# Kernel tuning notes

Measured on AMD Instinct MI355X. Metric: run time of the kernel, lower is better.

## Reference

```python
import jax, jax.numpy as jnp
import numpy as np

# plane_axes buffer from the torch module (permutation matrices)
PLANE_AXES = jnp.array([[[0, 1, 0], [1, 0, 0], [0, 0, 1]],
                        [[0, 0, 1], [1, 0, 0], [0, 1, 0]],
                        [[0, 1, 0], [0, 0, 1], [1, 0, 0]]], dtype=jnp.float32)

M = 1_000_000
C = 32
R = 512


def setup_inputs() -> dict:
    key = jax.random.key(0)
    k1, k2 = jax.random.split(key)
    # query points uniform in [-1, 1]^3 (grid_sample coordinate convention)
    xyz = jax.random.uniform(k1, (M, 3), dtype=jnp.float32) * 2.0 - 1.0
    triplane = jax.random.normal(k2, (1, 3, C, R, R), dtype=jnp.float32) * 0.05
    return {"xyz": xyz, "triplane": triplane, "oid": 0}


def _grid_sample_plane(img, gx, gy):
    """Bilinear grid_sample, align_corners=True, padding_mode='zeros'.
    img: [C, H, W]; gx, gy: [M] normalized coords in [-1, 1] (x -> W, y -> H).
    Returns [C, M]."""
    _, H, W = img.shape
    x = (gx + 1.0) * 0.5 * (W - 1)  # align_corners=True unnormalization
    y = (gy + 1.0) * 0.5 * (H - 1)
    x0 = jnp.floor(x)
    y0 = jnp.floor(y)
    x1 = x0 + 1.0
    y1 = y0 + 1.0
    wx1 = x - x0
    wx0 = 1.0 - wx1
    wy1 = y - y0
    wy0 = 1.0 - wy1

    def corner(xi, yi, w):
        valid = (xi >= 0) & (xi <= W - 1) & (yi >= 0) & (yi <= H - 1)
        xi_c = jnp.clip(xi, 0, W - 1).astype(jnp.int32)
        yi_c = jnp.clip(yi, 0, H - 1).astype(jnp.int32)
        vals = img[:, yi_c, xi_c]  # [C, M] gather
        return vals * (w * valid)[None, :]

    return (corner(x0, y0, wx0 * wy0) + corner(x1, y0, wx1 * wy0)
            + corner(x0, y1, wx0 * wy1) + corner(x1, y1, wx1 * wy1))


def reference(xyz, triplane, oid):
    # project_onto_planes: xyz [M,3] -> projections [3, M, 2]
    inv_planes = jnp.linalg.inv(PLANE_AXES)           # [3, 3, 3]
    proj = jnp.einsum('mk,pkj->pmj', xyz, inv_planes)[..., :2]  # [3, M, 2]
    planes = triplane[oid]                            # [3, C, R, R]
    # grid coords: last dim is (x, y) per torch grid_sample convention
    sampled = jax.vmap(_grid_sample_plane)(planes, proj[..., 0], proj[..., 1])  # [3, C, M]
    # permute(0,3,2,1).reshape(3,M,C).sum(0) -> [M, C]
    return sampled.sum(0).T
```

## Files before the change

### kernel.cpp

```cpp
#include <hip/hip_runtime.h>
#include <hip/hip_bf16.h>


#define RRTP 262144
#define CTP  32
#define NB   512
#define SORT_P 4096
#define TPBLK 3072
#define PLANE_B (RRTP * 64)

typedef float        f32x4 __attribute__((ext_vector_type(4)));
typedef unsigned int u32;
typedef u32          u32x4 __attribute__((ext_vector_type(4)));

__device__ __forceinline__ u32 part3b(u32 v) {
    return (v & 1) | ((v & 2) << 2) | ((v & 4) << 4);
}
__device__ __forceinline__ u32 morton9(float px, float py, float pz) {
    int qx = max(0, min(7, (int)((px + 1.0f) * 4.0f)));
    int qy = max(0, min(7, (int)((py + 1.0f) * 4.0f)));
    int qz = max(0, min(7, (int)((pz + 1.0f) * 4.0f)));
    return part3b((u32)qx) | (part3b((u32)qy) << 1) | (part3b((u32)qz) << 2);
}

__global__ __launch_bounds__(256) void tp_fused(const float* __restrict__ in,
                                                u32* __restrict__ texels,
                                                const float* __restrict__ xyz,
                                                u32* __restrict__ hist,
                                                const int* __restrict__ oid, int Mtot) {
    __shared__ float tile[256][33];
    const int t = threadIdx.x;

    if (blockIdx.x < TPBLK) {
        const int b     = blockIdx.x;
        const int plane = b >> 10;
        const int rr0   = (b & 1023) << 8;

        const float* src = in + (size_t)oid[0] * (3u * CTP * RRTP)
                              + (size_t)plane * (CTP * RRTP) + rr0 + t;
        #pragma unroll
        for (int c = 0; c < 32; ++c)
            tile[t][c] = src[(size_t)c * RRTP];
        __syncthreads();

        u32* dst = texels + (size_t)plane * ((size_t)RRTP * 16) + (size_t)rr0 * 16;
        const int cp = t & 15;
        #pragma unroll
        for (int k = 0; k < 16; ++k) {
            const int r = (k << 4) + (t >> 4);
            const float f0 = tile[r][cp * 2];
            const float f1 = tile[r][cp * 2 + 1];
            const u32 lo = (u32)__bfloat16_as_ushort(__float2bfloat16(f0));
            const u32 hi = (u32)__bfloat16_as_ushort(__float2bfloat16(f1));
            dst[(size_t)r * 16 + cp] = (hi << 16) | lo;
        }
    } else {
        u32* cnt = (u32*)&tile[0][0];
        const int b = blockIdx.x - TPBLK;
        cnt[t] = 0u; cnt[t + 256] = 0u;
        __syncthreads();
        const int base_m = b * SORT_P;
        #pragma unroll
        for (int i = 0; i < 16; ++i) {
            const int m = base_m + i * 256 + t;
            if (m < Mtot) {
                const u32 k = morton9(xyz[3 * m], xyz[3 * m + 1], xyz[3 * m + 2]);
                atomicAdd(&cnt[k], 1u);
            }
        }
        __syncthreads();
        hist[b * NB + t] = cnt[t];
        hist[b * NB + t + 256] = cnt[t + 256];
    }
}

__global__ __launch_bounds__(512) void tp_scanB(u32* __restrict__ hist,
                                                u32* __restrict__ bucket_base, int nblk) {
    const int k = threadIdx.x;
    u32 run = 0;
    #pragma unroll 8
    for (int b = 0; b < nblk; ++b) {
        const u32 v = hist[b * NB + k];
        hist[b * NB + k] = run;
        run += v;
    }
    __shared__ u32 sA[NB], sB[NB];
    sA[k] = run;
    int par = 0;
    for (int off = 1; off < NB; off <<= 1) {
        __syncthreads();
        u32* src = par ? sB : sA;
        u32* dst = par ? sA : sB;
        dst[k] = src[k] + ((k >= off) ? src[k - off] : 0u);
        par ^= 1;
    }
    __syncthreads();
    const u32 incl = (par ? sB : sA)[k];
    bucket_base[k] = incl - run;
}

__global__ __launch_bounds__(256) void tp_scatter_blk(const float* __restrict__ xyz,
                                                      const u32* __restrict__ hist,
                                                      const u32* __restrict__ bucket_base,
                                                      f32x4* __restrict__ sorted, int Mtot) {
    __shared__ u32 goff[NB];
    __shared__ u32 sA[NB], sB[NB];
    __shared__ f32x4 rec[SORT_P];
    __shared__ unsigned short lkey[SORT_P];
    const int t = threadIdx.x, b = blockIdx.x;
    const int base_m = b * SORT_P;

    sA[t] = 0u; sA[t + 256] = 0u;
    goff[t]       = bucket_base[t]       + hist[b * NB + t];
    goff[t + 256] = bucket_base[t + 256] + hist[b * NB + t + 256];
    __syncthreads();

    float xs[16], ys[16], zs[16]; u32 ks[16], rs[16];
    #pragma unroll
    for (int i = 0; i < 16; ++i) {
        const int m = base_m + i * 256 + t;
        const bool v = (m < Mtot);
        float px = 0.f, py = 0.f, pz = 0.f;
        if (v) { px = xyz[3 * m]; py = xyz[3 * m + 1]; pz = xyz[3 * m + 2]; }
        const u32 key = morton9(px, py, pz);
        xs[i] = px; ys[i] = py; zs[i] = pz;
        ks[i] = v ? key : 0xffffffffu;
        rs[i] = v ? atomicAdd(&sA[key], 1u) : 0u;
    }
    __syncthreads();

    const u32 c0 = sA[t], c1 = sA[t + 256];
    int par = 0;
    for (int off = 1; off < NB; off <<= 1) {
        u32* src = par ? sB : sA;
        u32* dst = par ? sA : sB;
        const u32 a0 = src[t]       + ((t >= off)       ? src[t - off]       : 0u);
        const u32 a1 = src[t + 256] + ((t + 256 >= off) ? src[t + 256 - off] : 0u);
        dst[t] = a0; dst[t + 256] = a1;
        par ^= 1;
        __syncthreads();
    }
    u32* incl = par ? sB : sA;
    const u32 lb0 = incl[t] - c0, lb1 = incl[t + 256] - c1;
    __syncthreads();
    sA[t] = lb0; sA[t + 256] = lb1;
    goff[t] -= lb0; goff[t + 256] -= lb1;
    __syncthreads();

    #pragma unroll
    for (int i = 0; i < 16; ++i) {
        if (ks[i] != 0xffffffffu) {
            const u32 pos = sA[ks[i]] + rs[i];
            f32x4 r = {xs[i], ys[i], zs[i],
                       __uint_as_float((u32)(base_m + i * 256 + t))};
            rec[pos] = r;
            lkey[pos] = (unsigned short)ks[i];
        }
    }
    __syncthreads();

    const int nv = min(SORT_P, Mtot - base_m);
    #pragma unroll
    for (int i = 0; i < 16; ++i) {
        const int s = i * 256 + t;
        if (s < nv) {
            const u32 k2 = lkey[s];
            sorted[goff[k2] + s] = rec[s];
        }
    }
}

__global__ __launch_bounds__(256) void tp_sample_sorted(const f32x4* __restrict__ sorted,
                                                        const u32* __restrict__ tp,
                                                        float* __restrict__ out,
                                                        int Mtot, int nwg) {
    __shared__ float srow[64][36];
    __shared__ u32   smid[64];

    const int bid = blockIdx.x;
    const int qc = nwg >> 3, rc = nwg & 7;
    const int xcd = bid & 7, j = bid >> 3;
    const int wg = ((xcd < rc) ? xcd * (qc + 1) : rc * (qc + 1) + (xcd - rc) * qc) + j;

    const int tid = wg * 256 + threadIdx.x;
    const int sp = tid >> 2;
    const u32 oq = (u32)((tid & 3) << 4);
    const int lp = threadIdx.x >> 2;

    if (sp < Mtot) {
        const f32x4 pt = sorted[sp];
        const float px = pt.x, py = pt.y, pz = pt.z;
        const u32 m = __float_as_uint(pt.w);

        const float gxs[3] = {py, pz, py};
        const float gys[3] = {px, px, pz};

        f32x4 alo = {0.f, 0.f, 0.f, 0.f};
        f32x4 ahi = {0.f, 0.f, 0.f, 0.f};

        const char* tpc = (const char*)tp;

        #pragma unroll
        for (int p = 0; p < 3; ++p) {
            const float xf = (gxs[p] + 1.0f) * (0.5f * 511.0f);
            const float yf = (gys[p] + 1.0f) * (0.5f * 511.0f);
            const float x0f = floorf(xf), y0f = floorf(yf);
            float wx1 = xf - x0f, wy1 = yf - y0f;
            float wx0 = 1.0f - wx1, wy0 = 1.0f - wy1;

            int x0 = (int)x0f, y0 = (int)y0f;
            int x1 = x0 + 1,   y1 = y0 + 1;
            if (x1 > 511) { x1 = 511; wx1 = 0.0f; }
            if (y1 > 511) { y1 = 511; wy1 = 0.0f; }
            x0 = max(0, min(511, x0));
            y0 = max(0, min(511, y0));

            const u32 ry0 = ((u32)y0 << 15), ry1 = ((u32)y1 << 15);
            const u32 cx0 = ((u32)x0 << 6)  + oq, cx1 = ((u32)x1 << 6) + oq;
            const char* base_p = tpc + (size_t)p * PLANE_B;

            const u32x4 v00 = *(const u32x4*)(base_p + (ry0 + cx0));
            const u32x4 v01 = *(const u32x4*)(base_p + (ry0 + cx1));
            const u32x4 v10 = *(const u32x4*)(base_p + (ry1 + cx0));
            const u32x4 v11 = *(const u32x4*)(base_p + (ry1 + cx1));

            const float w00 = wy0 * wx0, w01 = wy0 * wx1;
            const float w10 = wy1 * wx0, w11 = wy1 * wx1;

            #pragma unroll
            for (int i = 0; i < 4; ++i) {
                const float l00 = __uint_as_float(v00[i] << 16), h00 = __uint_as_float(v00[i] & 0xffff0000u);
                const float l01 = __uint_as_float(v01[i] << 16), h01 = __uint_as_float(v01[i] & 0xffff0000u);
                const float l10 = __uint_as_float(v10[i] << 16), h10 = __uint_as_float(v10[i] & 0xffff0000u);
                const float l11 = __uint_as_float(v11[i] << 16), h11 = __uint_as_float(v11[i] & 0xffff0000u);
                alo[i] = fmaf(w00, l00, fmaf(w01, l01, fmaf(w10, l10, fmaf(w11, l11, alo[i]))));
                ahi[i] = fmaf(w00, h00, fmaf(w01, h01, fmaf(w10, h10, fmaf(w11, h11, ahi[i]))));
            }
        }

        float* sr = &srow[lp][oq >> 1];
        sr[0] = alo[0]; sr[1] = ahi[0]; sr[2] = alo[1]; sr[3] = ahi[1];
        sr[4] = alo[2]; sr[5] = ahi[2]; sr[6] = alo[3]; sr[7] = ahi[3];
        smid[lp] = m;
    }
    __syncthreads();

    const int pc = threadIdx.x & 7;
    const int pb = threadIdx.x >> 3;
    const int spbase = wg * 64;
    #pragma unroll
    for (int jj = 0; jj < 2; ++jj) {
        const int lpt = pb + jj * 32;
        if (spbase + lpt < Mtot) {
            const u32 mj = smid[lpt];
            const f32x4 v = *(const f32x4*)&srow[lpt][pc << 2];
            __builtin_nontemporal_store(v, (f32x4*)(out + ((size_t)mj << 5) + (pc << 2)));
        }
    }
}

__global__ __launch_bounds__(256) void tp_sample_direct(const float* __restrict__ xyz,
                                                        const float* __restrict__ tpl,
                                                        const int* __restrict__ oid,
                                                        float* __restrict__ out,
                                                        int Mtot) {
    const int tid = blockIdx.x * 256 + threadIdx.x;
    const int m = tid >> 5;
    if (m >= Mtot) return;
    const int c = tid & 31;
    const float px = xyz[m * 3 + 0], py = xyz[m * 3 + 1], pz = xyz[m * 3 + 2];
    const float gxs[3] = {py, pz, py};
    const float gys[3] = {px, px, pz};
    const float* base = tpl + (size_t)oid[0] * (3u * CTP * RRTP);
    float acc = 0.f;
    #pragma unroll
    for (int p = 0; p < 3; ++p) {
        const float xf = (gxs[p] + 1.0f) * (0.5f * 511.0f);
        const float yf = (gys[p] + 1.0f) * (0.5f * 511.0f);
        const float x0f = floorf(xf), y0f = floorf(yf);
        float wx1 = xf - x0f, wy1 = yf - y0f;
        float wx0 = 1.0f - wx1, wy0 = 1.0f - wy1;
        int x0 = (int)x0f, y0 = (int)y0f;
        int x1 = x0 + 1,   y1 = y0 + 1;
        if (x1 > 511) { x1 = 511; wx1 = 0.0f; }
        if (y1 > 511) { y1 = 511; wy1 = 0.0f; }
        x0 = max(0, min(511, x0));
        y0 = max(0, min(511, y0));
        const float* img = base + ((size_t)p * CTP + c) * RRTP;
        acc += wy0 * (wx0 * img[(y0 << 9) + x0] + wx1 * img[(y0 << 9) + x1])
             + wy1 * (wx0 * img[(y1 << 9) + x0] + wx1 * img[(y1 << 9) + x1]);
    }
    out[((size_t)m << 5) + c] = acc;
}

extern "C" void kernel_launch(void* const* d_in, const int* in_sizes, int n_in,
                              void* d_out, int out_size, void* d_ws, size_t ws_size,
                              hipStream_t stream) {
    const float* xyz      = (const float*)d_in[0];
    const float* triplane = (const float*)d_in[1];
    const int*   oid      = (const int*)d_in[2];
    float*       out      = (float*)d_out;
    const int Mtot = in_sizes[0] / 3;
    const int nblk = (Mtot + SORT_P - 1) / SORT_P;

    const size_t hist_b   = 512 * 1024;
    const size_t bb_off   = hist_b;
    const size_t sorted_off = hist_b + 64 * 1024;
    const size_t sorted_b = (size_t)Mtot * 16;
    const size_t texel_off = sorted_off + sorted_b;
    const size_t texel_b  = (size_t)3 * RRTP * 16 * 4;
    const size_t ws_needed = texel_off + texel_b;

    if (ws_size >= ws_needed && (size_t)nblk * NB * 4 <= hist_b) {
        u32*   hist   = (u32*)d_ws;
        u32*   bbase  = (u32*)((char*)d_ws + bb_off);
        f32x4* sorted = (f32x4*)((char*)d_ws + sorted_off);
        u32*   texels = (u32*)((char*)d_ws + texel_off);

        tp_fused<<<TPBLK + nblk, 256, 0, stream>>>(triplane, texels, xyz, hist, oid, Mtot);
        tp_scanB<<<1, 512, 0, stream>>>(hist, bbase, nblk);
        tp_scatter_blk<<<nblk, 256, 0, stream>>>(xyz, hist, bbase, sorted, Mtot);

        const int nwg = (Mtot * 4 + 255) / 256;
        tp_sample_sorted<<<nwg, 256, 0, stream>>>(sorted, texels, out, Mtot, nwg);
    } else {
        tp_sample_direct<<<(Mtot * 32 + 255) / 256, 256, 0, stream>>>(xyz, triplane, oid, out, Mtot);
    }
}
```

Measured before the change: 135.8 us.

## Move triplane bf16 repack into the scatter kernel and halve sort block size

The triplane transpose/bf16 conversion now runs in the same launch as the per-block counting-sort scatter, not alongside the histogram pass. This keeps the serial histogram/scan phase short and lets the heavy repack overlap with the scatter. SORT_P is halved to 2048, giving more, lighter scatter blocks with a 40KB shared buffer reused across both roles. The cost is a larger histogram and a longer serial loop in the single-block scan (twice as many blocks).

```diff
diff --git a/kernel.cpp b/kernel.cpp
--- a/kernel.cpp
+++ b/kernel.cpp
@@ -5,7 +5,7 @@
 #define RRTP 262144
 #define CTP  32
 #define NB   512
-#define SORT_P 4096
+#define SORT_P 2048
 #define TPBLK 3072
 #define PLANE_B (RRTP * 64)
 
@@ -23,55 +23,24 @@
     return part3b((u32)qx) | (part3b((u32)qy) << 1) | (part3b((u32)qz) << 2);
 }
 
-__global__ __launch_bounds__(256) void tp_fused(const float* __restrict__ in,
-                                                u32* __restrict__ texels,
-                                                const float* __restrict__ xyz,
-                                                u32* __restrict__ hist,
-                                                const int* __restrict__ oid, int Mtot) {
-    __shared__ float tile[256][33];
-    const int t = threadIdx.x;
-
-    if (blockIdx.x < TPBLK) {
-        const int b     = blockIdx.x;
-        const int plane = b >> 10;
-        const int rr0   = (b & 1023) << 8;
-
-        const float* src = in + (size_t)oid[0] * (3u * CTP * RRTP)
-                              + (size_t)plane * (CTP * RRTP) + rr0 + t;
-        #pragma unroll
-        for (int c = 0; c < 32; ++c)
-            tile[t][c] = src[(size_t)c * RRTP];
-        __syncthreads();
-
-        u32* dst = texels + (size_t)plane * ((size_t)RRTP * 16) + (size_t)rr0 * 16;
-        const int cp = t & 15;
-        #pragma unroll
-        for (int k = 0; k < 16; ++k) {
-            const int r = (k << 4) + (t >> 4);
-            const float f0 = tile[r][cp * 2];
-            const float f1 = tile[r][cp * 2 + 1];
-            const u32 lo = (u32)__bfloat16_as_ushort(__float2bfloat16(f0));
-            const u32 hi = (u32)__bfloat16_as_ushort(__float2bfloat16(f1));
-            dst[(size_t)r * 16 + cp] = (hi << 16) | lo;
-        }
-    } else {
-        u32* cnt = (u32*)&tile[0][0];
-        const int b = blockIdx.x - TPBLK;
-        cnt[t] = 0u; cnt[t + 256] = 0u;
-        __syncthreads();
-        const int base_m = b * SORT_P;
-        #pragma unroll
-        for (int i = 0; i < 16; ++i) {
-            const int m = base_m + i * 256 + t;
-            if (m < Mtot) {
-                const u32 k = morton9(xyz[3 * m], xyz[3 * m + 1], xyz[3 * m + 2]);
-                atomicAdd(&cnt[k], 1u);
-            }
-        }
-        __syncthreads();
-        hist[b * NB + t] = cnt[t];
-        hist[b * NB + t + 256] = cnt[t + 256];
-    }
+__global__ __launch_bounds__(256) void tp_hist_blk(const float* __restrict__ xyz,
+                                                   u32* __restrict__ hist, int Mtot) {
+    __shared__ u32 cnt[NB];
+    const int t = threadIdx.x, b = blockIdx.x;
+    cnt[t] = 0u; cnt[t + 256] = 0u;
+    __syncthreads();
+    const int base_m = b * SORT_P;
+    #pragma unroll
+    for (int i = 0; i < 8; ++i) {
+        const int m = base_m + i * 256 + t;
+        if (m < Mtot) {
+            const u32 k = morton9(xyz[3 * m], xyz[3 * m + 1], xyz[3 * m + 2]);
+            atomicAdd(&cnt[k], 1u);
+        }
+    }
+    __syncthreads();
+    hist[b * NB + t] = cnt[t];
+    hist[b * NB + t + 256] = cnt[t + 256];
 }
 
 __global__ __launch_bounds__(512) void tp_scanB(u32* __restrict__ hist,
@@ -99,73 +68,108 @@
     bucket_base[k] = incl - run;
 }
 
-__global__ __launch_bounds__(256) void tp_scatter_blk(const float* __restrict__ xyz,
-                                                      const u32* __restrict__ hist,
-                                                      const u32* __restrict__ bucket_base,
-                                                      f32x4* __restrict__ sorted, int Mtot) {
-    __shared__ u32 goff[NB];
-    __shared__ u32 sA[NB], sB[NB];
-    __shared__ f32x4 rec[SORT_P];
-    __shared__ unsigned short lkey[SORT_P];
-    const int t = threadIdx.x, b = blockIdx.x;
-    const int base_m = b * SORT_P;
-
-    sA[t] = 0u; sA[t + 256] = 0u;
-    goff[t]       = bucket_base[t]       + hist[b * NB + t];
-    goff[t + 256] = bucket_base[t + 256] + hist[b * NB + t + 256];
-    __syncthreads();
-
-    float xs[16], ys[16], zs[16]; u32 ks[16], rs[16];
-    #pragma unroll
-    for (int i = 0; i < 16; ++i) {
-        const int m = base_m + i * 256 + t;
-        const bool v = (m < Mtot);
-        float px = 0.f, py = 0.f, pz = 0.f;
-        if (v) { px = xyz[3 * m]; py = xyz[3 * m + 1]; pz = xyz[3 * m + 2]; }
-        const u32 key = morton9(px, py, pz);
-        xs[i] = px; ys[i] = py; zs[i] = pz;
-        ks[i] = v ? key : 0xffffffffu;
-        rs[i] = v ? atomicAdd(&sA[key], 1u) : 0u;
-    }
-    __syncthreads();
-
-    const u32 c0 = sA[t], c1 = sA[t + 256];
-    int par = 0;
-    for (int off = 1; off < NB; off <<= 1) {
-        u32* src = par ? sB : sA;
-        u32* dst = par ? sA : sB;
-        const u32 a0 = src[t]       + ((t >= off)       ? src[t - off]       : 0u);
-        const u32 a1 = src[t + 256] + ((t + 256 >= off) ? src[t + 256 - off] : 0u);
-        dst[t] = a0; dst[t + 256] = a1;
-        par ^= 1;
-        __syncthreads();
-    }
-    u32* incl = par ? sB : sA;
-    const u32 lb0 = incl[t] - c0, lb1 = incl[t + 256] - c1;
-    __syncthreads();
-    sA[t] = lb0; sA[t + 256] = lb1;
-    goff[t] -= lb0; goff[t + 256] -= lb1;
-    __syncthreads();
-
-    #pragma unroll
-    for (int i = 0; i < 16; ++i) {
-        if (ks[i] != 0xffffffffu) {
-            const u32 pos = sA[ks[i]] + rs[i];
-            f32x4 r = {xs[i], ys[i], zs[i],
-                       __uint_as_float((u32)(base_m + i * 256 + t))};
-            rec[pos] = r;
-            lkey[pos] = (unsigned short)ks[i];
-        }
-    }
-    __syncthreads();
-
-    const int nv = min(SORT_P, Mtot - base_m);
-    #pragma unroll
-    for (int i = 0; i < 16; ++i) {
-        const int s = i * 256 + t;
-        if (s < nv) {
-            const u32 k2 = lkey[s];
-            sorted[goff[k2] + s] = rec[s];
+__global__ __launch_bounds__(256) void tp_fused2(const float* __restrict__ in,
+                                                 u32* __restrict__ texels,
+                                                 const float* __restrict__ xyz,
+                                                 const u32* __restrict__ hist,
+                                                 const u32* __restrict__ bucket_base,
+                                                 f32x4* __restrict__ sorted,
+                                                 const int* __restrict__ oid,
+                                                 int Mtot, int nscat) {
+    __shared__ alignas(16) char smem[40960];
+    const int t = threadIdx.x;
+
+    if (blockIdx.x >= nscat) {
+        float (*tile)[33] = (float(*)[33])smem;
+        const int b     = blockIdx.x - nscat;
+        const int plane = b >> 10;
+        const int rr0   = (b & 1023) << 8;
+
+        const float* src = in + (size_t)oid[0] * (3u * CTP * RRTP)
+                              + (size_t)plane * (CTP * RRTP) + rr0 + t;
+        #pragma unroll
+        for (int c = 0; c < 32; ++c)
+            tile[t][c] = src[(size_t)c * RRTP];
+        __syncthreads();
+
+        u32* dst = texels + (size_t)plane * ((size_t)RRTP * 16) + (size_t)rr0 * 16;
+        const int cp = t & 15;
+        #pragma unroll
+        for (int k = 0; k < 16; ++k) {
+            const int r = (k << 4) + (t >> 4);
+            const float f0 = tile[r][cp * 2];
+            const float f1 = tile[r][cp * 2 + 1];
+            const u32 lo = (u32)__bfloat16_as_ushort(__float2bfloat16(f0));
+            const u32 hi = (u32)__bfloat16_as_ushort(__float2bfloat16(f1));
+            dst[(size_t)r * 16 + cp] = (hi << 16) | lo;
+        }
+    } else {
+        f32x4* rec  = (f32x4*)smem;
+        u32*   goff = (u32*)(smem + 32768);
+        u32*   sA   = (u32*)(smem + 34816);
+        u32*   sB   = (u32*)(smem + 36864);
+        unsigned short* lkey = (unsigned short*)(smem + 36864);
+
+        const int b = blockIdx.x;
+        const int base_m = b * SORT_P;
+
+        sA[t] = 0u; sA[t + 256] = 0u;
+        goff[t]       = bucket_base[t]       + hist[b * NB + t];
+        goff[t + 256] = bucket_base[t + 256] + hist[b * NB + t + 256];
+        __syncthreads();
+
+        float xs[8], ys[8], zs[8]; u32 ks[8], rs[8];
+        #pragma unroll
+        for (int i = 0; i < 8; ++i) {
+            const int m = base_m + i * 256 + t;
+            const bool v = (m < Mtot);
+            float px = 0.f, py = 0.f, pz = 0.f;
+            if (v) { px = xyz[3 * m]; py = xyz[3 * m + 1]; pz = xyz[3 * m + 2]; }
+            const u32 key = morton9(px, py, pz);
+            xs[i] = px; ys[i] = py; zs[i] = pz;
+            ks[i] = v ? key : 0xffffffffu;
+            rs[i] = v ? atomicAdd(&sA[key], 1u) : 0u;
+        }
+        __syncthreads();
+
+        const u32 c0 = sA[t], c1 = sA[t + 256];
+        int par = 0;
+        for (int off = 1; off < NB; off <<= 1) {
+            u32* srcp = par ? sB : sA;
+            u32* dstp = par ? sA : sB;
+            const u32 a0 = srcp[t]       + ((t >= off)       ? srcp[t - off]       : 0u);
+            const u32 a1 = srcp[t + 256] + ((t + 256 >= off) ? srcp[t + 256 - off] : 0u);
+            dstp[t] = a0; dstp[t + 256] = a1;
+            par ^= 1;
+            __syncthreads();
+        }
+        u32* incl = par ? sB : sA;
+        const u32 lb0 = incl[t] - c0, lb1 = incl[t + 256] - c1;
+        __syncthreads();
+        sA[t] = lb0; sA[t + 256] = lb1;
+        goff[t] -= lb0; goff[t + 256] -= lb1;
+        __syncthreads();
+
+        #pragma unroll
+        for (int i = 0; i < 8; ++i) {
+            if (ks[i] != 0xffffffffu) {
+                const u32 pos = sA[ks[i]] + rs[i];
+                f32x4 r = {xs[i], ys[i], zs[i],
+                           __uint_as_float((u32)(base_m + i * 256 + t))};
+                rec[pos] = r;
+                lkey[pos] = (unsigned short)ks[i];
+            }
+        }
+        __syncthreads();
+
+        const int nv = min(SORT_P, Mtot - base_m);
+        #pragma unroll
+        for (int i = 0; i < 8; ++i) {
+            const int s = i * 256 + t;
+            if (s < nv) {
+                const u32 k2 = lkey[s];
+                sorted[goff[k2] + s] = rec[s];
+            }
         }
     }
 }
@@ -303,9 +307,9 @@
     const int Mtot = in_sizes[0] / 3;
     const int nblk = (Mtot + SORT_P - 1) / SORT_P;
 
-    const size_t hist_b   = 512 * 1024;
+    const size_t hist_b   = 1024 * 1024;
     const size_t bb_off   = hist_b;
-    const size_t sorted_off = hist_b + 64 * 1024;
+    const size_t sorted_off = hist_b + 16 * 1024;
     const size_t sorted_b = (size_t)Mtot * 16;
     const size_t texel_off = sorted_off + sorted_b;
     const size_t texel_b  = (size_t)3 * RRTP * 16 * 4;
@@ -317,9 +321,10 @@
         f32x4* sorted = (f32x4*)((char*)d_ws + sorted_off);
         u32*   texels = (u32*)((char*)d_ws + texel_off);
 
-        tp_fused<<<TPBLK + nblk, 256, 0, stream>>>(triplane, texels, xyz, hist, oid, Mtot);
+        tp_hist_blk<<<nblk, 256, 0, stream>>>(xyz, hist, Mtot);
         tp_scanB<<<1, 512, 0, stream>>>(hist, bbase, nblk);
-        tp_scatter_blk<<<nblk, 256, 0, stream>>>(xyz, hist, bbase, sorted, Mtot);
+        tp_fused2<<<nblk + TPBLK, 256, 0, stream>>>(triplane, texels, xyz, hist,
+                                                    bbase, sorted, oid, Mtot, nblk);
 
         const int nwg = (Mtot * 4 + 255) / 256;
         tp_sample_sorted<<<nwg, 256, 0, stream>>>(sorted, texels, out, Mtot, nwg);
```

After: 151.2 us. 1.11x slower.
